# Optimization experiments

Measured on AMD Instinct MI355X. Metric: run time of the kernel, lower is better.

Reference implementation:

```python
import jax, jax.numpy as jnp
import numpy as np

TOP_K = 1000
CROP_H, CROP_W = 14, 14
CANONICAL_SIZE = 224.0
CANONICAL_LEVEL = 1.0
MIN_LEVEL, MAX_LEVEL = 0, 4
EPS = 1e-7


def _crop_and_resize(image, boxes, crop_h, crop_w):
    """TF-style crop_and_resize (bilinear, extrapolation_value=0).
    image: [H, W, C]; boxes: [K, 4] normalized (y1, x1, y2, x2). -> [K, ch, cw, C]."""
    H, W, C = image.shape
    y1, x1, y2, x2 = boxes[:, 0], boxes[:, 1], boxes[:, 2], boxes[:, 3]
    Hs = jnp.asarray(H - 1, image.dtype)
    Ws = jnp.asarray(W - 1, image.dtype)
    ty = jnp.arange(crop_h, dtype=image.dtype) / (crop_h - 1)
    tx = jnp.arange(crop_w, dtype=image.dtype) / (crop_w - 1)
    iy = (y1[:, None] + ty[None, :] * (y2 - y1)[:, None]) * Hs  # [K, ch]
    ix = (x1[:, None] + tx[None, :] * (x2 - x1)[:, None]) * Ws  # [K, cw]
    y0f = jnp.floor(iy)
    x0f = jnp.floor(ix)
    ly = (iy - y0f)[:, :, None, None]
    lx = (ix - x0f)[:, None, :, None]
    y0 = jnp.clip(y0f, 0, H - 1).astype(jnp.int32)
    y1i = jnp.clip(y0f + 1, 0, H - 1).astype(jnp.int32)
    x0 = jnp.clip(x0f, 0, W - 1).astype(jnp.int32)
    x1i = jnp.clip(x0f + 1, 0, W - 1).astype(jnp.int32)

    def gather2(yi, xi):  # yi:[K,ch] xi:[K,cw] -> [K,ch,cw,C]
        return image[yi[:, :, None], xi[:, None, :]]

    tl = gather2(y0, x0)
    tr = gather2(y0, x1i)
    bl = gather2(y1i, x0)
    br = gather2(y1i, x1i)
    top = tl + (tr - tl) * lx
    bot = bl + (br - bl) * lx
    val = top + (bot - top) * ly
    valid = (((iy >= 0) & (iy <= Hs))[:, :, None, None]
             & ((ix >= 0) & (ix <= Ws))[:, None, :, None])
    return jnp.where(valid, val, jnp.zeros((), image.dtype))


def _forward(image_shape, detections, p3, p4, p5, p6, p7):
    det = detections[0]                       # [N, 4+num_classes]
    fpn = [p3[0], p4[0], p5[0], p6[0], p7[0]]  # each [Hi, Wi, C]
    # top-k by max class score (order differs from TF sorted=False, math identical)
    scores = jnp.max(det[:, 4:], axis=1)
    _, idx = jax.lax.top_k(scores, TOP_K)
    det = det[idx]
    # map to FPN level
    w = det[:, 2] - det[:, 0]
    h = det[:, 3] - det[:, 1]
    size = jnp.sqrt(w * h)
    levels = jnp.floor(CANONICAL_LEVEL + jnp.log2(size / CANONICAL_SIZE + EPS))
    levels = jnp.clip(levels, MIN_LEVEL, MAX_LEVEL).astype(jnp.int32)
    # the original concatenates per-level groups in order == stable sort by level
    order = jnp.argsort(levels, stable=True)
    det = det[order]
    levels = levels[order]
    img_h = image_shape[1].astype(det.dtype)
    img_w = image_shape[2].astype(det.dtype)
    boxes = jnp.stack([det[:, 1] / img_h, det[:, 0] / img_w,
                       det[:, 3] / img_h, det[:, 2] / img_w], axis=1)  # [K,4] y1x1y2x2
    C = fpn[0].shape[-1]
    rois = jnp.zeros((TOP_K, CROP_H, CROP_W, C), det.dtype)
    for i, fmap in enumerate(fpn):
        crops = _crop_and_resize(fmap, boxes, CROP_H, CROP_W)
        mask = (levels == i)[:, None, None, None]
        rois = rois + jnp.where(mask, crops, jnp.zeros((), det.dtype))
    return det[None], rois[None]


def setup_inputs() -> dict:
    key = jax.random.key(0)
    ks = jax.random.split(key, 8)
    N, NUM_CLASSES = 2000, 80
    IMG = 800.0
    x1 = jax.random.uniform(ks[0], (1, N)) * 600.0
    y1 = jax.random.uniform(ks[1], (1, N)) * 600.0
    w = jax.random.uniform(ks[2], (1, N)) * 192.0 + 8.0
    h = jax.random.uniform(ks[3], (1, N)) * 192.0 + 8.0
    x2 = jnp.minimum(x1 + w, IMG - 1.0)
    y2 = jnp.minimum(y1 + h, IMG - 1.0)
    cls = jax.random.uniform(ks[4], (1, N, NUM_CLASSES))
    detections = jnp.concatenate(
        [jnp.stack([x1, y1, x2, y2], axis=-1), cls], axis=-1).astype(jnp.float32)
    sizes = [100, 50, 25, 13, 7]
    fpn = [jax.random.normal(jax.random.fold_in(ks[5], i), (1, s, s, 256),
                             dtype=jnp.float32) for i, s in enumerate(sizes)]
    image_shape = jnp.array([1, 800, 800, 3], dtype=jnp.int32)
    return {"image_shape": image_shape, "detections": detections,
            "p3": fpn[0], "p4": fpn[1], "p5": fpn[2], "p6": fpn[3], "p7": fpn[4]}


def reference(image_shape, detections, p3, p4, p5, p6, p7):
    return _forward(image_shape, detections, p3, p4, p5, p6, p7)
```

## Files before the change

### kernel.cpp

```cpp
#include <hip/hip_runtime.h>
#include <math.h>

#define N_DET 2000
#define DET_STRIDE 84
#define TOPK 1000
#define CROP 14
#define C_CH 256
#define CROP_BLOCKS (TOPK * CROP * CROP / 8)
#define DET_BLOCKS ((TOPK * DET_STRIDE + 255) / 256)

typedef float nfloat4 __attribute__((ext_vector_type(4)));

__global__ __launch_bounds__(256) void k_score_level(
    const float* __restrict__ det,
    float* __restrict__ scores, int* __restrict__ levels) {
    int w = blockIdx.x * 4 + (threadIdx.x >> 6);
    int lane = threadIdx.x & 63;
    if (w >= N_DET) return;
    const float* row = det + (size_t)w * DET_STRIDE;
    float s = row[4 + lane];
    if (lane < 16) s = fmaxf(s, row[68 + lane]);
    #pragma unroll
    for (int m = 32; m >= 1; m >>= 1) s = fmaxf(s, __shfl_xor(s, m));
    if (lane == 0) {
        float bw = row[2] - row[0];
        float bh = row[3] - row[1];
        float sz = sqrtf(bw * bh);
        float lv = floorf(1.0f + log2f(sz / 224.0f + 1e-7f));
        lv = fminf(fmaxf(lv, 0.0f), 4.0f);
        scores[w] = s;
        levels[w] = (int)lv;
    }
}

__global__ __launch_bounds__(256) void k_rank(
    const float* __restrict__ scores, const int* __restrict__ levels,
    int* __restrict__ sel, int* __restrict__ levsel) {
    int t = blockIdx.x * 4 + (threadIdx.x >> 6);
    int lane = threadIdx.x & 63;
    if (t >= N_DET) return;
    float mine = scores[t];
    int cnt = 0;
    for (int j = lane; j < N_DET; j += 64) {
        float v = scores[j];
        cnt += (v > mine) || (v == mine && j < t);
    }
    #pragma unroll
    for (int m = 32; m >= 1; m >>= 1) cnt += __shfl_xor(cnt, m);
    if (lane == 0 && cnt < TOPK) {
        sel[cnt] = t;
        levsel[cnt] = levels[t];
    }
}

__global__ __launch_bounds__(256) void k_sort(
    const int* __restrict__ sel, const int* __restrict__ levsel,
    const float* __restrict__ det, const int* __restrict__ ishape,
    int* __restrict__ didx, int* __restrict__ lvl,
    float4* __restrict__ nbox) {
    int r = blockIdx.x * 4 + (threadIdx.x >> 6);
    int lane = threadIdx.x & 63;
    if (r >= TOPK) return;
    int myl = levsel[r];
    int pos = 0;
    for (int j = lane; j < TOPK; j += 64) {
        int lj = levsel[j];
        pos += (lj < myl) || (lj == myl && j < r);
    }
    #pragma unroll
    for (int m = 32; m >= 1; m >>= 1) pos += __shfl_xor(pos, m);
    if (lane == 0) {
        int di = sel[r];
        didx[pos] = di;
        lvl[pos] = myl;
        const float* drow = det + (size_t)di * DET_STRIDE;
        float imw = (float)ishape[2];
        float imh = (float)ishape[1];
        float4 nb;
        nb.x = drow[0] / imw;
        nb.y = drow[1] / imh;
        nb.z = drow[2] / imw;
        nb.w = drow[3] / imh;
        nbox[pos] = nb;
    }
}

__global__ __launch_bounds__(256) void k_crop(
    const float4* __restrict__ nbox, const int* __restrict__ lvl,
    const int* __restrict__ didx, const float* __restrict__ det,
    const float* __restrict__ p3, const float* __restrict__ p4,
    const float* __restrict__ p5, const float* __restrict__ p6,
    const float* __restrict__ p7,
    float* __restrict__ detout, float* __restrict__ rois) {
    if (blockIdx.x >= CROP_BLOCKS) {
        int e = (blockIdx.x - CROP_BLOCKS) * 256 + threadIdx.x;
        if (e < TOPK * DET_STRIDE) {
            int pos = e / DET_STRIDE;
            int col = e - pos * DET_STRIDE;
            detout[e] = det[(size_t)didx[pos] * DET_STRIDE + col];
        }
        return;
    }
    int w = blockIdx.x * 4 + (threadIdx.x >> 6);
    int lane = threadIdx.x & 63;
    int p0 = w * 2;
    int k = p0 / (CROP * CROP);
    int rem = p0 - k * (CROP * CROP);
    int yyA = rem / CROP;
    int xxA = rem - yyA * CROP;
    int remB = rem + 1;
    int yyB = remB / CROP;
    int xxB = remB - yyB * CROP;

    float4 nb = nbox[k];
    int level = lvl[k];
    int S;
    const float* fmap;
    switch (level) {
        case 0:  S = 100; fmap = p3; break;
        case 1:  S = 50;  fmap = p4; break;
        case 2:  S = 25;  fmap = p5; break;
        case 3:  S = 13;  fmap = p6; break;
        default: S = 7;   fmap = p7; break;
    }
    float Hs = (float)(S - 1);

    float tyA = (float)yyA / (float)(CROP - 1);
    float txA = (float)xxA / (float)(CROP - 1);
    float iyA = (nb.y + tyA * (nb.w - nb.y)) * Hs;
    float ixA = (nb.x + txA * (nb.z - nb.x)) * Hs;
    float y0fA = floorf(iyA), x0fA = floorf(ixA);
    float lyA = iyA - y0fA, lxA = ixA - x0fA;
    int y0A  = (int)fminf(fmaxf(y0fA,        0.0f), Hs);
    int y1A  = (int)fminf(fmaxf(y0fA + 1.0f, 0.0f), Hs);
    int x0A  = (int)fminf(fmaxf(x0fA,        0.0f), Hs);
    int x1A  = (int)fminf(fmaxf(x0fA + 1.0f, 0.0f), Hs);
    bool validA = (iyA >= 0.0f) & (iyA <= Hs) & (ixA >= 0.0f) & (ixA <= Hs);

    float tyB = (float)yyB / (float)(CROP - 1);
    float txB = (float)xxB / (float)(CROP - 1);
    float iyB = (nb.y + tyB * (nb.w - nb.y)) * Hs;
    float ixB = (nb.x + txB * (nb.z - nb.x)) * Hs;
    float y0fB = floorf(iyB), x0fB = floorf(ixB);
    float lyB = iyB - y0fB, lxB = ixB - x0fB;
    int y0B  = (int)fminf(fmaxf(y0fB,        0.0f), Hs);
    int y1B  = (int)fminf(fmaxf(y0fB + 1.0f, 0.0f), Hs);
    int x0B  = (int)fminf(fmaxf(x0fB,        0.0f), Hs);
    int x1B  = (int)fminf(fmaxf(x0fB + 1.0f, 0.0f), Hs);
    bool validB = (iyB >= 0.0f) & (iyB <= Hs) & (ixB >= 0.0f) & (ixB <= Hs);

    const float4* tlA = (const float4*)(fmap + ((size_t)y0A * S + x0A) * C_CH);
    const float4* trA = (const float4*)(fmap + ((size_t)y0A * S + x1A) * C_CH);
    const float4* blA = (const float4*)(fmap + ((size_t)y1A * S + x0A) * C_CH);
    const float4* brA = (const float4*)(fmap + ((size_t)y1A * S + x1A) * C_CH);
    const float4* tlB = (const float4*)(fmap + ((size_t)y0B * S + x0B) * C_CH);
    const float4* trB = (const float4*)(fmap + ((size_t)y0B * S + x1B) * C_CH);
    const float4* blB = (const float4*)(fmap + ((size_t)y1B * S + x0B) * C_CH);
    const float4* brB = (const float4*)(fmap + ((size_t)y1B * S + x1B) * C_CH);

    float4 a0 = tlA[lane], a1 = trA[lane], a2 = blA[lane], a3 = brA[lane];
    float4 b0 = tlB[lane], b1 = trB[lane], b2 = blB[lane], b3 = brB[lane];

    float4 oA, oB;
    #define LERP1(f, a, b, c, d, lx, ly)                   \
        { float tp = a.f + (b.f - a.f) * lx;               \
          float bt = c.f + (d.f - c.f) * lx;               \
          float r_ = tp + (bt - tp) * ly;                  \
          outv.f = r_; }
    {
        float4 outv;
        LERP1(x, a0, a1, a2, a3, lxA, lyA)
        LERP1(y, a0, a1, a2, a3, lxA, lyA)
        LERP1(z, a0, a1, a2, a3, lxA, lyA)
        LERP1(w, a0, a1, a2, a3, lxA, lyA)
        oA = outv;
    }
    {
        float4 outv;
        LERP1(x, b0, b1, b2, b3, lxB, lyB)
        LERP1(y, b0, b1, b2, b3, lxB, lyB)
        LERP1(z, b0, b1, b2, b3, lxB, lyB)
        LERP1(w, b0, b1, b2, b3, lxB, lyB)
        oB = outv;
    }
    #undef LERP1
    if (!validA) oA = make_float4(0.0f, 0.0f, 0.0f, 0.0f);
    if (!validB) oB = make_float4(0.0f, 0.0f, 0.0f, 0.0f);

    nfloat4 nA = { oA.x, oA.y, oA.z, oA.w };
    nfloat4 nB = { oB.x, oB.y, oB.z, oB.w };
    nfloat4* outA = (nfloat4*)(rois + (size_t)p0 * C_CH) + lane;
    nfloat4* outB = (nfloat4*)(rois + (size_t)(p0 + 1) * C_CH) + lane;
    __builtin_nontemporal_store(nA, outA);
    __builtin_nontemporal_store(nB, outB);
}

extern "C" void kernel_launch(void* const* d_in, const int* in_sizes, int n_in,
                              void* d_out, int out_size, void* d_ws, size_t ws_size,
                              hipStream_t stream) {
    const int* ishape  = (const int*)d_in[0];
    const float* det   = (const float*)d_in[1];
    const float* p3    = (const float*)d_in[2];
    const float* p4    = (const float*)d_in[3];
    const float* p5    = (const float*)d_in[4];
    const float* p6    = (const float*)d_in[5];
    const float* p7    = (const float*)d_in[6];
    float* out = (float*)d_out;

    float4* nbox = (float4*)d_ws;
    float* fbase = (float*)d_ws + 4 * TOPK;
    float* scores = fbase;
    int* levels = (int*)(fbase + N_DET);
    int* sel    = levels + N_DET;
    int* levsel = sel + TOPK;
    int* didx   = levsel + TOPK;
    int* lvl    = didx + TOPK;

    hipLaunchKernelGGL(k_score_level, dim3((N_DET + 3) / 4), dim3(256), 0, stream,
                       det, scores, levels);
    hipLaunchKernelGGL(k_rank, dim3((N_DET + 3) / 4), dim3(256), 0, stream,
                       scores, levels, sel, levsel);
    hipLaunchKernelGGL(k_sort, dim3((TOPK + 3) / 4), dim3(256), 0, stream,
                       sel, levsel, det, ishape, didx, lvl, nbox);
    hipLaunchKernelGGL(k_crop, dim3(CROP_BLOCKS + DET_BLOCKS), dim3(256), 0, stream,
                       nbox, lvl, didx, det, p3, p4, p5, p6, p7,
                       out, out + TOPK * DET_STRIDE);
}
```

Baseline: 258.6 us.

## Map crop blocks per box with XCD-aware ordering and four positions per wave

```diff
diff --git a/kernel.cpp b/kernel.cpp
--- a/kernel.cpp
+++ b/kernel.cpp
@@ -6,7 +6,11 @@
 #define TOPK 1000
 #define CROP 14
 #define C_CH 256
-#define CROP_BLOCKS (TOPK * CROP * CROP / 8)
+#define POS_PER_BOX (CROP * CROP)
+#define POS_PER_WAVE 4
+#define POS_PER_BLOCK 16
+#define BLOCKS_PER_BOX 13
+#define CROP_BLOCKS (TOPK * BLOCKS_PER_BOX)
 #define DET_BLOCKS ((TOPK * DET_STRIDE + 255) / 256)
 
 typedef float nfloat4 __attribute__((ext_vector_type(4)));
@@ -101,16 +105,15 @@
         }
         return;
     }
-    int w = blockIdx.x * 4 + (threadIdx.x >> 6);
-    int lane = threadIdx.x & 63;
-    int p0 = w * 2;
-    int k = p0 / (CROP * CROP);
-    int rem = p0 - k * (CROP * CROP);
-    int yyA = rem / CROP;
-    int xxA = rem - yyA * CROP;
-    int remB = rem + 1;
-    int yyB = remB / CROP;
-    int xxB = remB - yyB * CROP;
+    int wv = threadIdx.x >> 6;
+    int lane = threadIdx.x & 63;
+    int b = blockIdx.x;
+    int xcd = b & 7;
+    int t = b >> 3;
+    int grp = t / BLOCKS_PER_BOX;
+    int ib = t - grp * BLOCKS_PER_BOX;
+    int k = grp * 8 + xcd;
+    int local0 = ib * POS_PER_BLOCK + wv * POS_PER_WAVE;
 
     float4 nb = nbox[k];
     int level = lvl[k];
@@ -125,74 +128,80 @@
     }
     float Hs = (float)(S - 1);
 
-    float tyA = (float)yyA / (float)(CROP - 1);
-    float txA = (float)xxA / (float)(CROP - 1);
-    float iyA = (nb.y + tyA * (nb.w - nb.y)) * Hs;
-    float ixA = (nb.x + txA * (nb.z - nb.x)) * Hs;
-    float y0fA = floorf(iyA), x0fA = floorf(ixA);
-    float lyA = iyA - y0fA, lxA = ixA - x0fA;
-    int y0A  = (int)fminf(fmaxf(y0fA,        0.0f), Hs);
-    int y1A  = (int)fminf(fmaxf(y0fA + 1.0f, 0.0f), Hs);
-    int x0A  = (int)fminf(fmaxf(x0fA,        0.0f), Hs);
-    int x1A  = (int)fminf(fmaxf(x0fA + 1.0f, 0.0f), Hs);
-    bool validA = (iyA >= 0.0f) & (iyA <= Hs) & (ixA >= 0.0f) & (ixA <= Hs);
-
-    float tyB = (float)yyB / (float)(CROP - 1);
-    float txB = (float)xxB / (float)(CROP - 1);
-    float iyB = (nb.y + tyB * (nb.w - nb.y)) * Hs;
-    float ixB = (nb.x + txB * (nb.z - nb.x)) * Hs;
-    float y0fB = floorf(iyB), x0fB = floorf(ixB);
-    float lyB = iyB - y0fB, lxB = ixB - x0fB;
-    int y0B  = (int)fminf(fmaxf(y0fB,        0.0f), Hs);
-    int y1B  = (int)fminf(fmaxf(y0fB + 1.0f, 0.0f), Hs);
-    int x0B  = (int)fminf(fmaxf(x0fB,        0.0f), Hs);
-    int x1B  = (int)fminf(fmaxf(x0fB + 1.0f, 0.0f), Hs);
-    bool validB = (iyB >= 0.0f) & (iyB <= Hs) & (ixB >= 0.0f) & (ixB <= Hs);
-
-    const float4* tlA = (const float4*)(fmap + ((size_t)y0A * S + x0A) * C_CH);
-    const float4* trA = (const float4*)(fmap + ((size_t)y0A * S + x1A) * C_CH);
-    const float4* blA = (const float4*)(fmap + ((size_t)y1A * S + x0A) * C_CH);
-    const float4* brA = (const float4*)(fmap + ((size_t)y1A * S + x1A) * C_CH);
-    const float4* tlB = (const float4*)(fmap + ((size_t)y0B * S + x0B) * C_CH);
-    const float4* trB = (const float4*)(fmap + ((size_t)y0B * S + x1B) * C_CH);
-    const float4* blB = (const float4*)(fmap + ((size_t)y1B * S + x0B) * C_CH);
-    const float4* brB = (const float4*)(fmap + ((size_t)y1B * S + x1B) * C_CH);
-
-    float4 a0 = tlA[lane], a1 = trA[lane], a2 = blA[lane], a3 = brA[lane];
-    float4 b0 = tlB[lane], b1 = trB[lane], b2 = blB[lane], b3 = brB[lane];
-
-    float4 oA, oB;
-    #define LERP1(f, a, b, c, d, lx, ly)                   \
-        { float tp = a.f + (b.f - a.f) * lx;               \
-          float bt = c.f + (d.f - c.f) * lx;               \
-          float r_ = tp + (bt - tp) * ly;                  \
-          outv.f = r_; }
-    {
-        float4 outv;
-        LERP1(x, a0, a1, a2, a3, lxA, lyA)
-        LERP1(y, a0, a1, a2, a3, lxA, lyA)
-        LERP1(z, a0, a1, a2, a3, lxA, lyA)
-        LERP1(w, a0, a1, a2, a3, lxA, lyA)
-        oA = outv;
-    }
-    {
-        float4 outv;
-        LERP1(x, b0, b1, b2, b3, lxB, lyB)
-        LERP1(y, b0, b1, b2, b3, lxB, lyB)
-        LERP1(z, b0, b1, b2, b3, lxB, lyB)
-        LERP1(w, b0, b1, b2, b3, lxB, lyB)
-        oB = outv;
-    }
-    #undef LERP1
-    if (!validA) oA = make_float4(0.0f, 0.0f, 0.0f, 0.0f);
-    if (!validB) oB = make_float4(0.0f, 0.0f, 0.0f, 0.0f);
-
-    nfloat4 nA = { oA.x, oA.y, oA.z, oA.w };
-    nfloat4 nB = { oB.x, oB.y, oB.z, oB.w };
-    nfloat4* outA = (nfloat4*)(rois + (size_t)p0 * C_CH) + lane;
-    nfloat4* outB = (nfloat4*)(rois + (size_t)(p0 + 1) * C_CH) + lane;
-    __builtin_nontemporal_store(nA, outA);
-    __builtin_nontemporal_store(nB, outB);
+    const float4* ptl[POS_PER_WAVE];
+    const float4* ptr_[POS_PER_WAVE];
+    const float4* pbl[POS_PER_WAVE];
+    const float4* pbr[POS_PER_WAVE];
+    float plx[POS_PER_WAVE], ply[POS_PER_WAVE];
+    bool plive[POS_PER_WAVE];
+    #pragma unroll
+    for (int j = 0; j < POS_PER_WAVE; ++j) {
+        int local = local0 + j;
+        bool live = local < POS_PER_BOX;
+        int lc = live ? local : 0;
+        int yy = lc / CROP;
+        int xx = lc - yy * CROP;
+        float ty = (float)yy / (float)(CROP - 1);
+        float tx = (float)xx / (float)(CROP - 1);
+        float iy = (nb.y + ty * (nb.w - nb.y)) * Hs;
+        float ix = (nb.x + tx * (nb.z - nb.x)) * Hs;
+        float y0f = floorf(iy), x0f = floorf(ix);
+        float ly = iy - y0f, lx = ix - x0f;
+        int y0  = (int)fminf(fmaxf(y0f,        0.0f), Hs);
+        int y1  = (int)fminf(fmaxf(y0f + 1.0f, 0.0f), Hs);
+        int x0  = (int)fminf(fmaxf(x0f,        0.0f), Hs);
+        int x1  = (int)fminf(fmaxf(x0f + 1.0f, 0.0f), Hs);
+        bool valid = (iy >= 0.0f) & (iy <= Hs) & (ix >= 0.0f) & (ix <= Hs);
+        ptl[j]  = (const float4*)(fmap + ((size_t)y0 * S + x0) * C_CH);
+        ptr_[j] = (const float4*)(fmap + ((size_t)y0 * S + x1) * C_CH);
+        pbl[j]  = (const float4*)(fmap + ((size_t)y1 * S + x0) * C_CH);
+        pbr[j]  = (const float4*)(fmap + ((size_t)y1 * S + x1) * C_CH);
+        plx[j] = lx;
+        ply[j] = ly;
+        plive[j] = live && valid;
+    }
+
+    float4 ctl[POS_PER_WAVE], ctr[POS_PER_WAVE], cbl[POS_PER_WAVE], cbr[POS_PER_WAVE];
+    #pragma unroll
+    for (int j = 0; j < POS_PER_WAVE; ++j) {
+        ctl[j] = ptl[j][lane];
+        ctr[j] = ptr_[j][lane];
+        cbl[j] = pbl[j][lane];
+        cbr[j] = pbr[j][lane];
+    }
+
+    #pragma unroll
+    for (int j = 0; j < POS_PER_WAVE; ++j) {
+        float lx = plx[j], ly = ply[j];
+        float4 o;
+        {
+            float tp = ctl[j].x + (ctr[j].x - ctl[j].x) * lx;
+            float bt = cbl[j].x + (cbr[j].x - cbl[j].x) * lx;
+            o.x = tp + (bt - tp) * ly;
+        }
+        {
+            float tp = ctl[j].y + (ctr[j].y - ctl[j].y) * lx;
+            float bt = cbl[j].y + (cbr[j].y - cbl[j].y) * lx;
+            o.y = tp + (bt - tp) * ly;
+        }
+        {
+            float tp = ctl[j].z + (ctr[j].z - ctl[j].z) * lx;
+            float bt = cbl[j].z + (cbr[j].z - cbl[j].z) * lx;
+            o.z = tp + (bt - tp) * ly;
+        }
+        {
+            float tp = ctl[j].w + (ctr[j].w - ctl[j].w) * lx;
+            float bt = cbl[j].w + (cbr[j].w - cbl[j].w) * lx;
+            o.w = tp + (bt - tp) * ly;
+        }
+        int local = local0 + j;
+        if (local < POS_PER_BOX) {
+            if (!plive[j]) o = make_float4(0.0f, 0.0f, 0.0f, 0.0f);
+            nfloat4 nv = { o.x, o.y, o.z, o.w };
+            nfloat4* outp = (nfloat4*)(rois + ((size_t)k * POS_PER_BOX + local) * C_CH) + lane;
+            __builtin_nontemporal_store(nv, outp);
+        }
+    }
 }
 
 extern "C" void kernel_launch(void* const* d_in, const int* in_sizes, int n_in,
```

Result: faster. 251.7 us (-2.7%).
